# Kernel tuning notes

Hardware: AMD Instinct MI355X
Metric: run time of the kernel (lower is better)

## Reference

```python
import jax, jax.numpy as jnp
import numpy as np

D_MODEL = 1024
N_HEADS = 16
MAX_SEQ_LEN = 2048

def setup_inputs() -> dict:
    key = jax.random.key(0)
    ks = jax.random.split(key, 4)
    B, L, D = 2, 2048, D_MODEL
    s = 0.02
    x = jax.random.normal(ks[0], (B, L, D), dtype=jnp.float32)
    qkv_w = jax.random.normal(ks[1], (D, 3 * D), dtype=jnp.float32) * s
    qkv_b = jnp.zeros((3 * D,), dtype=jnp.float32)
    proj_w = jax.random.normal(ks[2], (D, D), dtype=jnp.float32) * s
    proj_b = jnp.zeros((D,), dtype=jnp.float32)
    bias_table = jax.random.normal(ks[3], (2 * MAX_SEQ_LEN - 1, N_HEADS), dtype=jnp.float32) * s
    return {"x": x, "qkv_w": qkv_w, "qkv_b": qkv_b, "proj_w": proj_w, "proj_b": proj_b, "bias_table": bias_table}

def reference(x, qkv_w, qkv_b, proj_w, proj_b, bias_table):
    B, L, D = x.shape
    H = N_HEADS
    dk = D // H
    scale = dk ** -0.5
    # fused qkv projection: (B,L,3,H,dk)
    qkv = (x @ qkv_w + qkv_b).reshape(B, L, 3, H, dk)
    q = qkv[:, :, 0].transpose(0, 2, 1, 3)  # (B,H,L,dk)
    k = qkv[:, :, 1].transpose(0, 2, 1, 3)
    v = qkv[:, :, 2].transpose(0, 2, 1, 3)
    attn = jnp.einsum("bhqd,bhkd->bhqk", q, k) * scale  # (B,H,L,L)
    # relative position bias gather (Swin-style)
    coords = jnp.arange(L)
    rel_idx = coords[None, :] - coords[:, None] + (MAX_SEQ_LEN - 1)  # (L,L)
    rel_bias = bias_table[rel_idx]  # (L,L,H)
    attn = attn + rel_bias.transpose(2, 0, 1)[None]  # (B,H,L,L)
    attn = jax.nn.softmax(attn, axis=-1)
    out = jnp.einsum("bhqk,bhkd->bhqd", attn, v)  # (B,H,L,dk)
    out = out.transpose(0, 2, 1, 3).reshape(B, L, D)
    return out @ proj_w + proj_b
```

## Files before the change

kernel.cpp:

```cpp
#include <hip/hip_runtime.h>
#include <stdint.h>

typedef __attribute__((ext_vector_type(4))) float    f32x4;
typedef f32x4 __attribute__((aligned(4)))   f32x4u;
typedef __attribute__((ext_vector_type(8))) short    bf16x8;
typedef __attribute__((ext_vector_type(2))) uint32_t u32x2;

#define MFMA16(a,b,c) __builtin_amdgcn_mfma_f32_16x16x32_bf16((a),(b),(c),0,0,0)

__device__ __forceinline__ uint16_t f2bf(float f){
  uint32_t u = __float_as_uint(f);
  return (uint16_t)((u + 0x7FFFu + ((u >> 16) & 1u)) >> 16);
}

__device__ __forceinline__ uint32_t pk_bf16(float lo, float hi){
  uint32_t r; asm("v_cvt_pk_bf16_f32 %0, %1, %2" : "=v"(r) : "v"(lo), "v"(hi)); return r;
}

__device__ __forceinline__ float fast_exp2(float x){
  float r; asm("v_exp_f32 %0, %1" : "=v"(r) : "v"(x)); return r;
}

__device__ __forceinline__ void gload16(const uint16_t* g, uint16_t* l){
  __builtin_amdgcn_global_load_lds((const __attribute__((address_space(1))) uint32_t*)g,
                                   (__attribute__((address_space(3))) uint32_t*)l, 16, 0, 0);
}

__global__ void k_cvtb(const float* __restrict__ in, uint16_t* __restrict__ out,
                       const float* __restrict__ btab, float* __restrict__ bias_t){
  const int bx = blockIdx.x;
  if (bx < 4096){
    const size_t i = (size_t)(bx*256 + threadIdx.x) * 4;
    const f32x4 v = *(const f32x4*)(in + i);
    u32x2 pk = {pk_bf16(v[0], v[1]), pk_bf16(v[2], v[3])};
    *(u32x2*)(out + i) = pk;
  } else {
    const int i = (bx - 4096)*256 + threadIdx.x;
    if (i < 4095*16) bias_t[(i & 15)*4096 + (i >> 4)] = btab[i] * 1.4426950408889634f;
  }
}

__global__ void k_tcvt(const float* __restrict__ in, uint16_t* __restrict__ out, int K, int N){
  __shared__ float tile[64][65];
  const int k0 = blockIdx.y*64, n0 = blockIdx.x*64;
  const int tc = threadIdx.x & 63, tr = threadIdx.x >> 6;
  #pragma unroll
  for (int p=0;p<16;p++){ int r = p*4 + tr; tile[r][tc] = in[(size_t)(k0+r)*N + n0 + tc]; }
  __syncthreads();
  #pragma unroll
  for (int p=0;p<16;p++){ int r = p*4 + tr; out[(size_t)(n0+r)*K + k0 + tc] = f2bf(tile[tc][r]); }
}

__global__ __launch_bounds__(256, 2) void k_gemm(
    const uint16_t* __restrict__ A, const uint16_t* __restrict__ Bt,
    const float* __restrict__ bias,
    uint16_t* __restrict__ qo, uint16_t* __restrict__ ko, uint16_t* __restrict__ vto)
{
  __shared__ __align__(16) uint16_t at[128*64];
  __shared__ __align__(16) uint16_t bt[128*64];
  const int tid = threadIdx.x;
  const int lane = tid & 63, w = tid >> 6;
  const int g = lane >> 4, li = lane & 15;
  const int wr = w >> 1, wc = w & 1;
  const int m0 = blockIdx.y * 128, n0 = blockIdx.x * 128;

  f32x4 acc[4][4] = {};

  const int srow = tid >> 3;
  const int scg  = (tid & 7) ^ (srow & 7);

  for (int kt_ = 0; kt_ < 16; kt_++){
    const int kk = kt_*64;
    __syncthreads();
    #pragma unroll
    for (int j = 0; j < 4; j++){
      gload16(A  + (size_t)(m0 + j*32 + srow)*1024 + kk + scg*8, at + (j*256+tid)*8);
      gload16(Bt + (size_t)(n0 + j*32 + srow)*1024 + kk + scg*8, bt + (j*256+tid)*8);
    }
    asm volatile("s_waitcnt vmcnt(0)" ::: "memory");
    __syncthreads();

    bf16x8 af[2][4], bfr[2][4];
    #pragma unroll
    for (int mi=0; mi<4; mi++){
      int row = wr*64 + mi*16 + li, sw = row & 7;
      af[0][mi] = *(const bf16x8*)(at + row*64 + ((g     ^ sw)*8));
      af[1][mi] = *(const bf16x8*)(at + row*64 + (((4+g) ^ sw)*8));
    }
    #pragma unroll
    for (int ni=0; ni<4; ni++){
      int row = wc*64 + ni*16 + li, sw = row & 7;
      bfr[0][ni] = *(const bf16x8*)(bt + row*64 + ((g     ^ sw)*8));
      bfr[1][ni] = *(const bf16x8*)(bt + row*64 + (((4+g) ^ sw)*8));
    }
    #pragma unroll
    for (int s=0; s<2; s++)
      #pragma unroll
      for (int mi=0; mi<4; mi++)
        #pragma unroll
        for (int ni=0; ni<4; ni++)
          acc[mi][ni] = MFMA16(af[s][mi], bfr[s][ni], acc[mi][ni]);
  }

  #pragma unroll
  for (int ni=0; ni<4; ni++){
    const int c = n0 + wc*64 + ni*16 + li;
    const float bv = bias[c];
    const int which = c >> 10, cc = c & 1023;
    const int h = cc >> 6, d = cc & 63;
    #pragma unroll
    for (int mi=0; mi<4; mi++){
      const int trow = m0 + wr*64 + mi*16 + g*4;
      const int b_ = trow >> 11, lcl = trow & 2047;
      const f32x4 v4 = acc[mi][ni];
      if (which == 0){
        uint16_t* dst = qo + (((size_t)(b_*16 + h)*2048 + lcl)*64 + d);
        #pragma unroll
        for (int r=0;r<4;r++) dst[(size_t)r*64] = f2bf((v4[r] + bv) * 0.18033688011112042f);
      } else if (which == 1){
        uint16_t* dst = ko + (((size_t)(b_*16 + h)*2048 + lcl)*64 + d);
        #pragma unroll
        for (int r=0;r<4;r++) dst[(size_t)r*64] = f2bf(v4[r] + bv);
      } else {
        u32x2 pk = {pk_bf16(v4[0]+bv, v4[1]+bv), pk_bf16(v4[2]+bv, v4[3]+bv)};
        *(u32x2*)(vto + (((size_t)(b_*16 + h)*64 + d)*2048 + lcl)) = pk;
      }
    }
  }
}

__global__ __launch_bounds__(256, 2) void k_gemm2(
    const uint16_t* __restrict__ A, const uint16_t* __restrict__ Bt,
    const float* __restrict__ bias, float* __restrict__ outf)
{
  __shared__ __align__(16) uint16_t at[128*64];
  __shared__ __align__(16) uint16_t bt[64*64];
  const int tid = threadIdx.x;
  const int lane = tid & 63, w = tid >> 6;
  const int g = lane >> 4, li = lane & 15;
  const int wr = w >> 1, wc = w & 1;
  const int m0 = blockIdx.y * 128, n0 = blockIdx.x * 64;

  f32x4 acc[4][2] = {};
  const int srow = tid >> 3;
  const int scg  = (tid & 7) ^ (srow & 7);

  for (int kt_ = 0; kt_ < 16; kt_++){
    const int kk = kt_*64;
    __syncthreads();
    #pragma unroll
    for (int j = 0; j < 4; j++)
      gload16(A  + (size_t)(m0 + j*32 + srow)*1024 + kk + scg*8, at + (j*256+tid)*8);
    #pragma unroll
    for (int j = 0; j < 2; j++)
      gload16(Bt + (size_t)(n0 + j*32 + srow)*1024 + kk + scg*8, bt + (j*256+tid)*8);
    asm volatile("s_waitcnt vmcnt(0)" ::: "memory");
    __syncthreads();

    bf16x8 af[2][4], bfr[2][2];
    #pragma unroll
    for (int mi=0; mi<4; mi++){
      int row = wr*64 + mi*16 + li, sw = row & 7;
      af[0][mi] = *(const bf16x8*)(at + row*64 + ((g     ^ sw)*8));
      af[1][mi] = *(const bf16x8*)(at + row*64 + (((4+g) ^ sw)*8));
    }
    #pragma unroll
    for (int ni=0; ni<2; ni++){
      int row = wc*32 + ni*16 + li, sw = row & 7;
      bfr[0][ni] = *(const bf16x8*)(bt + row*64 + ((g     ^ sw)*8));
      bfr[1][ni] = *(const bf16x8*)(bt + row*64 + (((4+g) ^ sw)*8));
    }
    #pragma unroll
    for (int s=0; s<2; s++)
      #pragma unroll
      for (int mi=0; mi<4; mi++)
        #pragma unroll
        for (int ni=0; ni<2; ni++)
          acc[mi][ni] = MFMA16(af[s][mi], bfr[s][ni], acc[mi][ni]);
  }

  #pragma unroll
  for (int ni=0; ni<2; ni++){
    const int c = n0 + wc*32 + ni*16 + li;
    const float bv = bias[c];
    #pragma unroll
    for (int mi=0; mi<4; mi++){
      const int trow = m0 + wr*64 + mi*16 + g*4;
      float* dst = outf + (size_t)trow*1024 + c;
      const f32x4 v4 = acc[mi][ni];
      #pragma unroll
      for (int r=0;r<4;r++) dst[(size_t)r*1024] = v4[r] + bv;
    }
  }
}

__device__ __forceinline__ void attn_tile(
    int t, bool last, int tid, int g, int li, int srow, int scg,
    const uint16_t* kbase, const uint16_t* vbase, const float* bb,
    const uint16_t* ktc, uint16_t* ktn, const uint16_t* vtc, uint16_t* vtn, uint16_t* pl,
    const bf16x8 (&qf)[2][2], bf16x8 ones,
    f32x4 (&o)[4][2], f32x4 (&o4)[2], float& mrun0, float& mrun1)
{
  const int kv0 = t*64;

  f32x4 bv5[5];
  #pragma unroll
  for (int j=0;j<5;j++)
    bv5[j] = *(const f32x4u*)(bb + kv0 + (j-1)*16 + g*4 - li);
  asm volatile("" ::: "memory");

  if (!last){
    const int kv1 = kv0 + 64;
    gload16(kbase + (size_t)(kv1+srow)*64 + scg*8,         ktn + tid*8);
    gload16(kbase + (size_t)(kv1+srow+32)*64 + scg*8,      ktn + 2048 + tid*8);
    gload16(vbase + (size_t)srow*2048 + kv1 + scg*8,       vtn + tid*8);
    gload16(vbase + (size_t)(srow+32)*2048 + kv1 + scg*8,  vtn + 2048 + tid*8);
    asm volatile("s_waitcnt vmcnt(9)" ::: "memory");
  } else {
    asm volatile("s_waitcnt vmcnt(5)" ::: "memory");
  }
  __builtin_amdgcn_s_barrier();

  f32x4 sa[4][2];
  __builtin_amdgcn_s_setprio(1);
  #pragma unroll
  for (int mf=0; mf<4; mf++){
    const int row = mf*16 + li, sw = row & 7;
    bf16x8 a0 = *(const bf16x8*)(ktc + row*64 + ((g     ^ sw)*8));
    bf16x8 a1 = *(const bf16x8*)(ktc + row*64 + (((4+g) ^ sw)*8));
    #pragma unroll
    for (int c=0;c<2;c++){
      f32x4 cfr = {};
      cfr = MFMA16(a0, qf[c][0], cfr);
      cfr = MFMA16(a1, qf[c][1], cfr);
      sa[mf][c] = cfr;
    }
  }
  __builtin_amdgcn_s_setprio(0);

  float t0 = -__builtin_inff(), t1 = -__builtin_inff();
  #pragma unroll
  for (int mf=0; mf<4; mf++){
    sa[mf][0] += bv5[mf+1];
    sa[mf][1] += bv5[mf];
    #pragma unroll
    for (int r=0; r<4; r++){
      t0 = fmaxf(t0, sa[mf][0][r]);
      t1 = fmaxf(t1, sa[mf][1][r]);
    }
  }

  const int ok = (t0 <= mrun0 + 8.f) && (t1 <= mrun1 + 8.f);
  if (!__all(ok)){
    float r0 = t0, r1 = t1;
    r0 = fmaxf(r0, __shfl_xor(r0, 16)); r0 = fmaxf(r0, __shfl_xor(r0, 32));
    r1 = fmaxf(r1, __shfl_xor(r1, 16)); r1 = fmaxf(r1, __shfl_xor(r1, 32));
    const float mn0 = fmaxf(mrun0, r0), mn1 = fmaxf(mrun1, r1);
    const float a0 = fast_exp2(mrun0 - mn0), a1 = fast_exp2(mrun1 - mn1);
    #pragma unroll
    for (int mf=0; mf<4; mf++){ o[mf][0] *= a0; o[mf][1] *= a1; }
    o4[0] *= a0; o4[1] *= a1;
    mrun0 = mn0; mrun1 = mn1;
  }

  bf16x8 av[2][4];
  #pragma unroll
  for (int s=0; s<2; s++)
    #pragma unroll
    for (int mf=0; mf<4; mf++){
      const int row = mf*16 + li, sw = row & 7;
      av[s][mf] = *(const bf16x8*)(vtc + row*64 + (((4*s+g) ^ sw)*8));
    }

  const int swp2 = 2*(li & 7);
  #pragma unroll
  for (int c=0;c<2;c++){
    const float mr = c ? mrun1 : mrun0;
    #pragma unroll
    for (int mf=0; mf<4; mf++){
      float p0 = fast_exp2(sa[mf][c][0] - mr);
      float p1 = fast_exp2(sa[mf][c][1] - mr);
      float p2 = fast_exp2(sa[mf][c][2] - mr);
      float p3 = fast_exp2(sa[mf][c][3] - mr);
      u32x2 pk = {pk_bf16(p0,p1), pk_bf16(p2,p3)};
      *(u32x2*)(pl + li*64 + (((4*mf+g) ^ swp2)*4)) = pk;
    }
    __builtin_amdgcn_s_setprio(1);
    #pragma unroll
    for (int s=0; s<2; s++){
      bf16x8 pb = *(const bf16x8*)(pl + li*64 + (((8*s+2*g) ^ swp2)*4));
      o4[c] = MFMA16(ones, pb, o4[c]);
      #pragma unroll
      for (int mf=0; mf<4; mf++)
        o[mf][c] = MFMA16(av[s][mf], pb, o[mf][c]);
    }
    __builtin_amdgcn_s_setprio(0);
  }
  __builtin_amdgcn_s_barrier();
}

__global__ __launch_bounds__(256, 2) void k_attn(
    const uint16_t* __restrict__ qg, const uint16_t* __restrict__ kg,
    const uint16_t* __restrict__ vg, const float* __restrict__ biast,
    uint16_t* __restrict__ outp)
{
  __shared__ __align__(16) uint16_t kt[2][64*64];
  __shared__ __align__(16) uint16_t vt[2][64*64];
  __shared__ __align__(16) uint16_t pt[4][16*64];
  const int tid = threadIdx.x;
  const int lane = tid & 63, w = tid >> 6;
  const int g = lane >> 4, li = lane & 15;
  const int bh = blockIdx.y, h = bh & 15, b_ = bh >> 4;
  const int qw = blockIdx.x*128 + w*32;

  bf16x8 qf[2][2];
  #pragma unroll
  for (int c=0;c<2;c++){
    const uint16_t* qp = qg + ((size_t)bh*2048 + qw + c*16 + li)*64 + g*8;
    qf[c][0] = *(const bf16x8*)(qp);
    qf[c][1] = *(const bf16x8*)(qp + 32);
  }
  bf16x8 ones = (bf16x8)(short)0;
  if (li == 0){ const short v = (short)0x3F80; ones = (bf16x8){v,v,v,v,v,v,v,v}; }

  f32x4 o[4][2] = {};
  f32x4 o4[2] = {};
  float mrun0 = -__builtin_inff(), mrun1 = -__builtin_inff();

  const uint16_t* kbase = kg + (size_t)bh*(2048*64);
  const uint16_t* vbase = vg + (size_t)bh*(64*2048);
  const int srow = tid >> 3;
  const int scg  = (tid & 7) ^ (srow & 7);
  const float* bb = biast + h*4096 + 2047 - qw;
  uint16_t* pl = &pt[w][0];

  gload16(kbase + (size_t)srow*64 + scg*8,         &kt[0][tid*8]);
  gload16(kbase + (size_t)(srow+32)*64 + scg*8,    &kt[0][2048 + tid*8]);
  gload16(vbase + (size_t)srow*2048 + scg*8,       &vt[0][tid*8]);
  gload16(vbase + (size_t)(srow+32)*2048 + scg*8,  &vt[0][2048 + tid*8]);

  for (int tt = 0; tt < 32; tt += 2){
    attn_tile(tt,   false,    tid, g, li, srow, scg, kbase, vbase, bb,
              &kt[0][0], &kt[1][0], &vt[0][0], &vt[1][0], pl,
              qf, ones, o, o4, mrun0, mrun1);
    attn_tile(tt+1, tt == 30, tid, g, li, srow, scg, kbase, vbase, bb,
              &kt[1][0], &kt[0][0], &vt[1][0], &vt[0][0], pl,
              qf, ones, o, o4, mrun0, mrun1);
  }

  const float ls0 = __shfl(o4[0][0], li);
  const float ls1 = __shfl(o4[1][0], li);
  const float inv0 = 1.0f / ls0, inv1 = 1.0f / ls1;
  #pragma unroll
  for (int c=0;c<2;c++){
    const float inv = c ? inv1 : inv0;
    const size_t token = (size_t)b_*2048 + qw + c*16 + li;
    #pragma unroll
    for (int mf=0; mf<4; mf++){
      u32x2 pk = {pk_bf16(o[mf][c][0]*inv, o[mf][c][1]*inv),
                  pk_bf16(o[mf][c][2]*inv, o[mf][c][3]*inv)};
      *(u32x2*)(outp + token*1024 + h*64 + mf*16 + g*4) = pk;
    }
  }
}

extern "C" void kernel_launch(void* const* d_in, const int* in_sizes, int n_in,
                              void* d_out, int out_size, void* d_ws, size_t ws_size,
                              hipStream_t stream)
{
  const float* x      = (const float*)d_in[0];
  const float* qkv_w  = (const float*)d_in[1];
  const float* qkv_b  = (const float*)d_in[2];
  const float* proj_w = (const float*)d_in[3];
  const float* proj_b = (const float*)d_in[4];
  const float* btab   = (const float*)d_in[5];
  float* out = (float*)d_out;

  char* p = (char*)d_ws;
  uint16_t* x_bf    = (uint16_t*)(p);
  uint16_t* qkv_wt  = (uint16_t*)(p + 8388608);
  uint16_t* proj_wt = (uint16_t*)(p + 14680064);
  uint16_t* q_buf   = (uint16_t*)(p + 16777216);
  uint16_t* k_buf   = (uint16_t*)(p + 25165824);
  uint16_t* vt_buf  = (uint16_t*)(p + 33554432);
  uint16_t* ao_buf  = (uint16_t*)(p + 41943040);
  float*    bias_t  = (float*)   (p + 50331648);

  k_cvtb <<<dim3(4352),  dim3(256), 0, stream>>>(x, x_bf, btab, bias_t);
  k_tcvt <<<dim3(48,16), dim3(256), 0, stream>>>(qkv_w,  qkv_wt,  1024, 3072);
  k_tcvt <<<dim3(16,16), dim3(256), 0, stream>>>(proj_w, proj_wt, 1024, 1024);

  k_gemm   <<<dim3(24,32), dim3(256), 0, stream>>>(x_bf, qkv_wt, qkv_b, q_buf, k_buf, vt_buf);
  k_attn   <<<dim3(16,32), dim3(256), 0, stream>>>(q_buf, k_buf, vt_buf, bias_t, ao_buf);
  k_gemm2  <<<dim3(16,32), dim3(256), 0, stream>>>(ao_buf, proj_wt, proj_b, out);
}
```

Measured before the change: 119.5 us.

## Merge preprocessing kernels into one launch and halve QKV GEMM M-tile

```diff
diff --git a/kernel.cpp b/kernel.cpp
--- a/kernel.cpp
+++ b/kernel.cpp
@@ -26,23 +26,34 @@
                                    (__attribute__((address_space(3))) uint32_t*)l, 16, 0, 0);
 }
 
-__global__ void k_cvtb(const float* __restrict__ in, uint16_t* __restrict__ out,
-                       const float* __restrict__ btab, float* __restrict__ bias_t){
+__global__ void k_prep(const float* __restrict__ x, uint16_t* __restrict__ x_bf,
+                       const float* __restrict__ btab, float* __restrict__ bias_t,
+                       const float* __restrict__ qkv_w, uint16_t* __restrict__ qkv_wt,
+                       const float* __restrict__ proj_w, uint16_t* __restrict__ proj_wt){
+  __shared__ float tile[64][65];
   const int bx = blockIdx.x;
   if (bx < 4096){
     const size_t i = (size_t)(bx*256 + threadIdx.x) * 4;
-    const f32x4 v = *(const f32x4*)(in + i);
+    const f32x4 v = *(const f32x4*)(x + i);
     u32x2 pk = {pk_bf16(v[0], v[1]), pk_bf16(v[2], v[3])};
-    *(u32x2*)(out + i) = pk;
-  } else {
+    *(u32x2*)(x_bf + i) = pk;
+    return;
+  }
+  if (bx < 4352){
     const int i = (bx - 4096)*256 + threadIdx.x;
     if (i < 4095*16) bias_t[(i & 15)*4096 + (i >> 4)] = btab[i] * 1.4426950408889634f;
-  }
-}
-
-__global__ void k_tcvt(const float* __restrict__ in, uint16_t* __restrict__ out, int K, int N){
-  __shared__ float tile[64][65];
-  const int k0 = blockIdx.y*64, n0 = blockIdx.x*64;
+    return;
+  }
+  const float* in;  uint16_t* out;  int K, N, n0, k0;
+  if (bx < 5120){
+    const int b2 = bx - 4352;
+    in = qkv_w; out = qkv_wt; K = 1024; N = 3072;
+    n0 = (b2 % 48)*64; k0 = (b2 / 48)*64;
+  } else {
+    const int b3 = bx - 5120;
+    in = proj_w; out = proj_wt; K = 1024; N = 1024;
+    n0 = (b3 % 16)*64; k0 = (b3 / 16)*64;
+  }
   const int tc = threadIdx.x & 63, tr = threadIdx.x >> 6;
   #pragma unroll
   for (int p=0;p<16;p++){ int r = p*4 + tr; tile[r][tc] = in[(size_t)(k0+r)*N + n0 + tc]; }
@@ -56,15 +67,14 @@
     const float* __restrict__ bias,
     uint16_t* __restrict__ qo, uint16_t* __restrict__ ko, uint16_t* __restrict__ vto)
 {
-  __shared__ __align__(16) uint16_t at[128*64];
+  __shared__ __align__(16) uint16_t at[64*64];
   __shared__ __align__(16) uint16_t bt[128*64];
   const int tid = threadIdx.x;
-  const int lane = tid & 63, w = tid >> 6;
+  const int lane = tid & 63, wc = tid >> 6;
   const int g = lane >> 4, li = lane & 15;
-  const int wr = w >> 1, wc = w & 1;
-  const int m0 = blockIdx.y * 128, n0 = blockIdx.x * 128;
-
-  f32x4 acc[4][4] = {};
+  const int m0 = blockIdx.y * 64, n0 = blockIdx.x * 128;
+
+  f32x4 acc[4][2] = {};
 
   const int srow = tid >> 3;
   const int scg  = (tid & 7) ^ (srow & 7);
@@ -73,23 +83,24 @@
     const int kk = kt_*64;
     __syncthreads();
     #pragma unroll
-    for (int j = 0; j < 4; j++){
+    for (int j = 0; j < 2; j++)
       gload16(A  + (size_t)(m0 + j*32 + srow)*1024 + kk + scg*8, at + (j*256+tid)*8);
+    #pragma unroll
+    for (int j = 0; j < 4; j++)
       gload16(Bt + (size_t)(n0 + j*32 + srow)*1024 + kk + scg*8, bt + (j*256+tid)*8);
-    }
     asm volatile("s_waitcnt vmcnt(0)" ::: "memory");
     __syncthreads();
 
-    bf16x8 af[2][4], bfr[2][4];
+    bf16x8 af[2][4], bfr[2][2];
     #pragma unroll
     for (int mi=0; mi<4; mi++){
-      int row = wr*64 + mi*16 + li, sw = row & 7;
+      int row = mi*16 + li, sw = row & 7;
       af[0][mi] = *(const bf16x8*)(at + row*64 + ((g     ^ sw)*8));
       af[1][mi] = *(const bf16x8*)(at + row*64 + (((4+g) ^ sw)*8));
     }
     #pragma unroll
-    for (int ni=0; ni<4; ni++){
-      int row = wc*64 + ni*16 + li, sw = row & 7;
+    for (int ni=0; ni<2; ni++){
+      int row = wc*32 + ni*16 + li, sw = row & 7;
       bfr[0][ni] = *(const bf16x8*)(bt + row*64 + ((g     ^ sw)*8));
       bfr[1][ni] = *(const bf16x8*)(bt + row*64 + (((4+g) ^ sw)*8));
     }
@@ -98,19 +109,19 @@
       #pragma unroll
       for (int mi=0; mi<4; mi++)
         #pragma unroll
-        for (int ni=0; ni<4; ni++)
+        for (int ni=0; ni<2; ni++)
           acc[mi][ni] = MFMA16(af[s][mi], bfr[s][ni], acc[mi][ni]);
   }
 
   #pragma unroll
-  for (int ni=0; ni<4; ni++){
-    const int c = n0 + wc*64 + ni*16 + li;
+  for (int ni=0; ni<2; ni++){
+    const int c = n0 + wc*32 + ni*16 + li;
     const float bv = bias[c];
     const int which = c >> 10, cc = c & 1023;
     const int h = cc >> 6, d = cc & 63;
     #pragma unroll
     for (int mi=0; mi<4; mi++){
-      const int trow = m0 + wr*64 + mi*16 + g*4;
+      const int trow = m0 + mi*16 + g*4;
       const int b_ = trow >> 11, lcl = trow & 2047;
       const f32x4 v4 = acc[mi][ni];
       if (which == 0){
@@ -386,11 +397,10 @@
   uint16_t* ao_buf  = (uint16_t*)(p + 41943040);
   float*    bias_t  = (float*)   (p + 50331648);
 
-  k_cvtb <<<dim3(4352),  dim3(256), 0, stream>>>(x, x_bf, btab, bias_t);
-  k_tcvt <<<dim3(48,16), dim3(256), 0, stream>>>(qkv_w,  qkv_wt,  1024, 3072);
-  k_tcvt <<<dim3(16,16), dim3(256), 0, stream>>>(proj_w, proj_wt, 1024, 1024);
-
-  k_gemm   <<<dim3(24,32), dim3(256), 0, stream>>>(x_bf, qkv_wt, qkv_b, q_buf, k_buf, vt_buf);
-  k_attn   <<<dim3(16,32), dim3(256), 0, stream>>>(q_buf, k_buf, vt_buf, bias_t, ao_buf);
-  k_gemm2  <<<dim3(16,32), dim3(256), 0, stream>>>(ao_buf, proj_wt, proj_b, out);
-}
+  k_prep <<<dim3(5376), dim3(256), 0, stream>>>(x, x_bf, btab, bias_t,
+                                                qkv_w, qkv_wt, proj_w, proj_wt);
+
+  k_gemm  <<<dim3(24,64), dim3(256), 0, stream>>>(x_bf, qkv_wt, qkv_b, q_buf, k_buf, vt_buf);
+  k_attn  <<<dim3(16,32), dim3(256), 0, stream>>>(q_buf, k_buf, vt_buf, bias_t, ao_buf);
+  k_gemm2 <<<dim3(16,32), dim3(256), 0, stream>>>(ao_buf, proj_wt, proj_b, out);
+}
```

After: 118.0 us (median of 2 runs). About the same (-1.2%).
